# Kernel tuning notes

Measured on AMD Instinct MI355X. Metric: run time of the kernel, lower is better.

Reference implementation:

```python
import jax, jax.numpy as jnp
import numpy as np

N, C, T, V = 32, 64, 256, 25
IC, NS = 16, 3  # inter_channels = C // 4, num_subset = 3
EPS = 1e-5


def _bn(x, g, b, m, v):
    # inference-mode BatchNorm2d over channel dim of [N, C, T, V]
    scale = g / jnp.sqrt(v + EPS)
    return (x - m[:, None, None]) * scale[:, None, None] + b[:, None, None]


def _conv1x1(x, w, b):
    # 1x1 Conv2d on [N, C, T, V]; w: [O, C], b: [O]
    return jnp.einsum('nctv,oc->notv', x, w) + b[None, :, None, None]


def setup_inputs() -> dict:
    key = jax.random.key(0)
    ks = iter(jax.random.split(key, 40))
    def nrm(shape, s=0.05):
        return jax.random.normal(next(ks), shape, jnp.float32) * s
    inp = {}
    inp['feature'] = jax.random.normal(next(ks), (N, C, T, V), jnp.float32)
    inp['hidden'] = jax.random.normal(next(ks), (N, C, T, V), jnp.float32)
    inp['A'] = jax.random.uniform(next(ks), (NS, V, V), jnp.float32) * 0.1
    inp['PA'] = jnp.full((NS, V, V), 1e-6, jnp.float32)
    inp['conv_a_w'] = nrm((NS, IC, C)); inp['conv_a_b'] = nrm((NS, IC))
    inp['conv_b_w'] = nrm((NS, IC, C)); inp['conv_b_b'] = nrm((NS, IC))
    inp['conv_d_w'] = nrm((NS, C, C));  inp['conv_d_b'] = nrm((NS, C))
    inp['gbn_g'] = 0.5 + jax.random.uniform(next(ks), (C,), jnp.float32)
    inp['gbn_b'] = nrm((C,))
    inp['gbn_m'] = nrm((C,))
    inp['gbn_v'] = 0.5 + jax.random.uniform(next(ks), (C,), jnp.float32)
    inp['tcn_w'] = nrm((C, C, 9, 1)); inp['tcn_b'] = nrm((C,))
    inp['tbn_g'] = 0.5 + jax.random.uniform(next(ks), (C,), jnp.float32)
    inp['tbn_b'] = nrm((C,))
    inp['tbn_m'] = nrm((C,))
    inp['tbn_v'] = 0.5 + jax.random.uniform(next(ks), (C,), jnp.float32)
    for nme in ['W_ir', 'W_ii', 'W_in', 'W_hr', 'W_hi', 'W_hh']:
        inp[nme] = nrm((C, C))
    for nme in ['b_ir', 'b_ii', 'b_in']:
        inp[nme] = nrm((C,))
    return inp


def _tcn_gcn(h, A, PA, caw, cab, cbw, cbb, cdw, cdb,
             gbn_g, gbn_b, gbn_m, gbn_v, tcn_w, tcn_b,
             tbn_g, tbn_b, tbn_m, tbn_v):
    # unit_gcn (in == out -> down is identity)
    Aeff = A + PA  # [NS, V, V]
    scale = 1.0 / (IC * T)
    y = 0.0
    h_flat = h.reshape(N, C * T, V)
    for i in range(NS):
        a = _conv1x1(h, caw[i], cab[i])            # [N, IC, T, V]
        b = _conv1x1(h, cbw[i], cbb[i])            # [N, IC, T, V]
        A1 = a.transpose(0, 3, 1, 2).reshape(N, V, IC * T)
        A2 = b.reshape(N, IC * T, V)
        att = jax.nn.softmax(jnp.einsum('nvk,nkw->nvw', A1, A2) * scale, axis=-2)
        att = att + Aeff[i]                         # [N, V, V]
        z = jnp.einsum('nkv,nvw->nkw', h_flat, att).reshape(N, C, T, V)
        y = y + _conv1x1(z, cdw[i], cdb[i])
    gcn_out = jax.nn.relu(_bn(y, gbn_g, gbn_b, gbn_m, gbn_v) + h)
    # unit_tcn: (9,1) conv, pad (4,0), stride 1
    t = jax.lax.conv_general_dilated(
        gcn_out, tcn_w, window_strides=(1, 1), padding=[(4, 4), (0, 0)],
        dimension_numbers=('NCHW', 'OIHW', 'NCHW'))
    t = t + tcn_b[None, :, None, None]
    t = _bn(t, tbn_g, tbn_b, tbn_m, tbn_v)
    # residual is identity (in==out, stride 1)
    return jax.nn.relu(t + h)


def reference(feature, hidden, A, PA, conv_a_w, conv_a_b, conv_b_w, conv_b_b,
              conv_d_w, conv_d_b, gbn_g, gbn_b, gbn_m, gbn_v, tcn_w, tcn_b,
              tbn_g, tbn_b, tbn_m, tbn_v, W_ir, b_ir, W_ii, b_ii, W_in, b_in,
              W_hr, W_hi, W_hh):
    msg = _tcn_gcn(hidden, A, PA, conv_a_w, conv_a_b, conv_b_w, conv_b_b,
                   conv_d_w, conv_d_b, gbn_g, gbn_b, gbn_m, gbn_v,
                   tcn_w, tcn_b, tbn_g, tbn_b, tbn_m, tbn_v)
    feat = feature.transpose(0, 2, 3, 1).reshape(N, T * V, C)
    msg2 = msg.transpose(0, 2, 3, 1).reshape(N, T * V, C)
    hid2 = hidden.transpose(0, 2, 3, 1).reshape(N, T * V, C)
    r = jax.nn.sigmoid(feat @ W_ir.T + b_ir + msg2 @ W_hr.T)
    z = jax.nn.sigmoid(feat @ W_ii.T + b_ii + msg2 @ W_hi.T)
    n = jnp.tanh(feat @ W_in.T + b_in + r * (msg2 @ W_hh.T))
    h_new = (1.0 - z) * n + z * hid2
    return h_new.reshape(N, T, V, C).transpose(0, 3, 1, 2)
```

## Files before the change

kernel.cpp:

```cpp
#include <hip/hip_runtime.h>
#include <math.h>

#define TV 6400
#define NTOT 32

typedef __attribute__((ext_vector_type(8))) short short8;
typedef __attribute__((ext_vector_type(4))) short short4v;
typedef __attribute__((ext_vector_type(4))) float f32x4;

__device__ __forceinline__ float b2f(short s) {
  unsigned u = ((unsigned)(unsigned short)s) << 16;
  return __uint_as_float(u);
}
__device__ __forceinline__ short f2b(float f) {
  unsigned u = __float_as_uint(f);
  u = (u + 0x7FFF + ((u >> 16) & 1)) >> 16;
  return (short)u;
}
__device__ __forceinline__ float fsig(float x) {
  return __builtin_amdgcn_rcpf(1.f + __expf(-x));
}
__device__ __forceinline__ float ftanh(float x) {
  float x2 = fminf(fmaxf(2.f * x, -80.f), 80.f);
  float t = __expf(x2);
  return (t - 1.f) * __builtin_amdgcn_rcpf(t + 1.f);
}

__global__ __launch_bounds__(256) void pack_kernel(
    const float* __restrict__ tcn_w, const float* __restrict__ caw,
    const float* __restrict__ cbw, const float* __restrict__ cdw,
    const float* __restrict__ W_ir, const float* __restrict__ W_ii,
    const float* __restrict__ W_in, const float* __restrict__ W_hr,
    const float* __restrict__ W_hi, const float* __restrict__ W_hh,
    const float* __restrict__ cab, const float* __restrict__ cbb,
    const float* __restrict__ b_ir, const float* __restrict__ b_ii,
    const float* __restrict__ b_in,
    short* __restrict__ P, float* __restrict__ Pb)
{
  int idx = blockIdx.x * 256 + threadIdx.x;
  if (idx < 9984) {
    int lane = idx & 63;
    int rest = idx >> 6;
    int c = rest & 1;
    rest >>= 1;
    int mloc = lane & 15, kb = c * 32 + (lane >> 4) * 8;
    short8 v;
    if (rest < 6) {
      int m = rest * 16 + mloc;
      for (int i = 0; i < 8; ++i)
        v[i] = f2b(m < 48 ? caw[m * 64 + kb + i] : cbw[(m - 48) * 64 + kb + i]);
    } else if (rest < 18) {
      int m = (rest - 6) * 16 + mloc;
      for (int i = 0; i < 8; ++i) v[i] = f2b(cdw[m * 64 + kb + i]);
    } else if (rest < 30) {
      int m = (rest - 18) * 16 + mloc;
      const float* W = (m < 64) ? W_ir : (m < 128 ? W_ii : W_in);
      int mr = m & 63;
      for (int i = 0; i < 8; ++i) v[i] = f2b(W[mr * 64 + kb + i]);
    } else if (rest < 42) {
      int m = (rest - 30) * 16 + mloc;
      const float* W = (m < 64) ? W_hr : (m < 128 ? W_hi : W_hh);
      int mr = m & 63;
      for (int i = 0; i < 8; ++i) v[i] = f2b(W[mr * 64 + kb + i]);
    } else {
      int t = rest - 42;
      int kk = t >> 2, mf = t & 3;
      int o = mf * 16 + mloc;
      for (int i = 0; i < 8; ++i) v[i] = f2b(tcn_w[o * 576 + (kb + i) * 9 + kk]);
    }
    *(short8*)(P + (size_t)idx * 8) = v;
  } else if (idx < 9984 + 288) {
    int r = idx - 9984;
    if (r < 96) Pb[r] = (r < 48) ? cab[r] : cbb[r - 48];
    else {
      int q = r - 96;
      Pb[r] = (q < 64) ? b_ir[q] : (q < 128 ? b_ii[q - 64] : b_in[q - 128]);
    }
  }
}

__global__ __launch_bounds__(256) void convert_kernel(
    const float* __restrict__ hid, const float* __restrict__ feat,
    short* __restrict__ hidK, short* __restrict__ featK)
{
  int j = blockIdx.x * 256 + threadIdx.x;
  int gy = blockIdx.y;
  int n = blockIdx.z;
  const float* src = ((gy < 8) ? hid : feat) + ((long)n * 64 + (long)(gy & 7) * 8) * TV + j;
  short* dst = ((gy < 8) ? hidK : featK) + (((long)n * 8 + (gy & 7)) * TV + j) * 8;
  short8 o;
#pragma unroll
  for (int i = 0; i < 8; ++i) o[i] = f2b(src[(long)i * TV]);
  *(short8*)dst = o;
}

__global__ __launch_bounds__(256) void ab_gemm(
    const short8* __restrict__ Wp, const short8* __restrict__ Bk,
    short* __restrict__ Cout, const float* __restrict__ bias)
{
  const int tid = threadIdx.x;
  const int lane = tid & 63, w = tid >> 6;
  const int q = lane >> 4, lj = lane & 15;
  const int j0 = blockIdx.x * 128;
  const int n = blockIdx.y;
  const short8* Bn = Bk + (long)n * 8 * TV;
  short* Cn = Cout + (long)n * 96 * TV;

  f32x4 acc[6][2];
  for (int a = 0; a < 6; ++a) for (int b = 0; b < 2; ++b)
    acc[a][b] = (f32x4){0.f, 0.f, 0.f, 0.f};

  for (int c = 0; c < 2; ++c) {
    short8 bf0 = Bn[(long)(c * 4 + q) * TV + j0 + (w * 2 + 0) * 16 + lj];
    short8 bf1 = Bn[(long)(c * 4 + q) * TV + j0 + (w * 2 + 1) * 16 + lj];
#pragma unroll
    for (int mf = 0; mf < 6; ++mf) {
      short8 af = Wp[(mf * 2 + c) * 64 + lane];
      acc[mf][0] = __builtin_amdgcn_mfma_f32_16x16x32_bf16(af, bf0, acc[mf][0], 0, 0, 0);
      acc[mf][1] = __builtin_amdgcn_mfma_f32_16x16x32_bf16(af, bf1, acc[mf][1], 0, 0, 0);
    }
  }
#pragma unroll
  for (int mf = 0; mf < 6; ++mf) {
    int k0 = mf * 16 + q * 4;
    int g = k0 >> 3, i0 = k0 & 7;
    float bv[4];
#pragma unroll
    for (int r = 0; r < 4; ++r) bv[r] = bias[k0 + r];
#pragma unroll
    for (int jf = 0; jf < 2; ++jf) {
      int j = j0 + (w * 2 + jf) * 16 + lj;
      short4v o4;
#pragma unroll
      for (int r = 0; r < 4; ++r) o4[r] = f2b(acc[mf][jf][r] + bv[r]);
      *(short4v*)(Cn + ((long)g * TV + j) * 8 + i0) = o4;
    }
  }
}

__global__ __launch_bounds__(256) void att_partial(
    const short* __restrict__ abK, float* __restrict__ partial)
{
  const int ch = blockIdx.x, i = blockIdx.y, n = blockIdx.z;
  __shared__ float sA[6400], sB[6400];
  const int tid = threadIdx.x;
  const long nb = (long)n * 96 * TV;
  const int t0 = ch * 16;
  for (int idx = tid; idx < 800; idx += 256) {
    int gh = idx / 400, jl = idx - gh * 400;
    long j = (long)t0 * 25 + jl;
    short8 va = *(const short8*)&abK[nb + ((long)(2 * i + gh) * TV + j) * 8];
    short8 vb = *(const short8*)&abK[nb + ((long)(6 + 2 * i + gh) * TV + j) * 8];
#pragma unroll
    for (int e = 0; e < 8; ++e) {
      sA[(gh * 8 + e) * 400 + jl] = b2f(va[e]);
      sB[(gh * 8 + e) * 400 + jl] = b2f(vb[e]);
    }
  }
  __syncthreads();
  const int a0 = tid >> 4, b0 = tid & 15;
  const int v1 = a0 + 16, w1 = b0 + 16;
  const int v1c = (v1 < 25) ? v1 : 0, w1c = (w1 < 25) ? w1 : 0;
  float acc00 = 0, acc01 = 0, acc10 = 0, acc11 = 0;
#pragma unroll 8
  for (int r = 0; r < 256; ++r) {
    float av0 = sA[r * 25 + a0], av1 = sA[r * 25 + v1c];
    float bw0 = sB[r * 25 + b0], bw1 = sB[r * 25 + w1c];
    acc00 += av0 * bw0; acc01 += av0 * bw1;
    acc10 += av1 * bw0; acc11 += av1 * bw1;
  }
  const float scale = 1.0f / 4096.0f;
  float* pp = partial + (((long)(n * 3 + i) * 16) + ch) * 625;
  pp[a0 * 25 + b0] = acc00 * scale;
  if (w1 < 25) pp[a0 * 25 + w1] = acc01 * scale;
  if (v1 < 25) pp[v1 * 25 + b0] = acc10 * scale;
  if (v1 < 25 && w1 < 25) pp[v1 * 25 + w1] = acc11 * scale;
}

__global__ __launch_bounds__(256) void att_reduce(
    const float* __restrict__ partial, const float* __restrict__ Amat,
    const float* __restrict__ PAmat, short* __restrict__ attP)
{
  const int i = blockIdx.x, n = blockIdx.y;
  __shared__ float sL[625];
  const int tid = threadIdx.x;
  const float* pp = partial + ((long)(n * 3 + i) * 16) * 625;
  for (int idx = tid; idx < 625; idx += 256) {
    float s = 0.f;
#pragma unroll
    for (int c = 0; c < 16; ++c) s += pp[c * 625 + idx];
    sL[idx] = s;
  }
  __syncthreads();
  if (tid < 25) {
    const int w = tid;
    float mx = -1e30f;
#pragma unroll
    for (int v = 0; v < 25; ++v) mx = fmaxf(mx, sL[v * 25 + w]);
    float e[25];
    float s = 0.f;
#pragma unroll
    for (int v = 0; v < 25; ++v) { e[v] = __expf(sL[v * 25 + w] - mx); s += e[v]; }
    float inv = 1.f / s;
#pragma unroll
    for (int v = 0; v < 25; ++v)
      sL[v * 25 + w] = e[v] * inv + Amat[i * 625 + v * 25 + w] + PAmat[i * 625 + v * 25 + w];
  }
  __syncthreads();
  if (tid < 128) {
    int wf = tid >> 6, lane = tid & 63;
    int q = lane >> 4, lj = lane & 15;
    int w = wf * 16 + lj;
    short8 o = {0, 0, 0, 0, 0, 0, 0, 0};
    if (w < 25) {
#pragma unroll
      for (int e2 = 0; e2 < 8; ++e2) {
        int v = q * 8 + e2;
        if (v < 25) o[e2] = f2b(sL[v * 25 + w]);
      }
    }
    *(short8*)(attP + (size_t)(((long)(n * 3 + i) * 2 + wf) * 64 + lane) * 8) = o;
  }
}

#define UST 136
#define OST 101
__global__ __launch_bounds__(256) void gcn_fused(
    const short8* __restrict__ Wu, const short8* __restrict__ attP,
    const short8* __restrict__ hidK, const float* __restrict__ cdb,
    const float* __restrict__ gg, const float* __restrict__ gb,
    const float* __restrict__ gm, const float* __restrict__ gv,
    short* __restrict__ gcnK)
{
  __shared__ __align__(16) short uT[192 * UST];
  __shared__ float A2[64], B2[64];
  short* sOut = uT;
  const int tid = threadIdx.x;
  if (tid < 64) {
    float sc = gg[tid] * rsqrtf(gv[tid] + 1e-5f);
    A2[tid] = sc;
    float bias = cdb[tid] + cdb[64 + tid] + cdb[128 + tid];
    B2[tid] = bias * sc + (gb[tid] - gm[tid] * sc);
  }
  for (int idx = tid; idx < 5376; idx += 256) {
    int row = idx / 28, rr = idx - row * 28;
    int g = rr / 7, s = 25 + (rr - g * 7);
    uT[row * UST + g * 32 + s] = 0;
  }
  const int lane = tid & 63, w = tid >> 6;
  const int q = lane >> 4, lj = lane & 15;
  const int tt = blockIdx.x, n = blockIdx.y;
  const int jb = tt * 100;
  const short8* Hn = hidK + (long)n * 8 * TV;

  f32x4 uacc[3][7];
  for (int a = 0; a < 3; ++a) for (int b = 0; b < 7; ++b)
    uacc[a][b] = (f32x4){0.f, 0.f, 0.f, 0.f};
  for (int c = 0; c < 2; ++c) {
    short8 bf[7];
#pragma unroll
    for (int jf = 0; jf < 7; ++jf)
      bf[jf] = Hn[(long)(c * 4 + q) * TV + jb + jf * 16 + lj];
#pragma unroll
    for (int ml = 0; ml < 3; ++ml) {
      short8 af = Wu[((w * 3 + ml) * 2 + c) * 64 + lane];
#pragma unroll
      for (int jf = 0; jf < 7; ++jf)
        uacc[ml][jf] = __builtin_amdgcn_mfma_f32_16x16x32_bf16(af, bf[jf], uacc[ml][jf], 0, 0, 0);
    }
  }
#pragma unroll
  for (int ml = 0; ml < 3; ++ml) {
    int row0 = (w * 3 + ml) * 16 + q * 4;
#pragma unroll
    for (int jf = 0; jf < 7; ++jf) {
      int col = jf * 16 + lj;
      if (col < 100) {
        int cc = (col / 25) * 32 + (col % 25);
#pragma unroll
        for (int r = 0; r < 4; ++r)
          uT[(row0 + r) * UST + cc] = f2b(uacc[ml][jf][r]);
      }
    }
  }
  __syncthreads();

  const int colt = w * 25;
  short8 attA[6];
#pragma unroll
  for (int i = 0; i < 3; ++i)
#pragma unroll
    for (int wf = 0; wf < 2; ++wf)
      attA[i * 2 + wf] = attP[((long)(n * 3 + i) * 2 + wf) * 64 + lane];

  f32x4 macc[2][4];
  for (int a = 0; a < 2; ++a) for (int b = 0; b < 4; ++b)
    macc[a][b] = (f32x4){0.f, 0.f, 0.f, 0.f};
#pragma unroll
  for (int i = 0; i < 3; ++i) {
#pragma unroll
    for (int of = 0; of < 4; ++of) {
      int row = i * 64 + of * 16 + lj;
      short8 bf = *(const short8*)&uT[row * UST + w * 32 + q * 8];
      macc[0][of] = __builtin_amdgcn_mfma_f32_16x16x32_bf16(attA[i * 2 + 0], bf, macc[0][of], 0, 0, 0);
      macc[1][of] = __builtin_amdgcn_mfma_f32_16x16x32_bf16(attA[i * 2 + 1], bf, macc[1][of], 0, 0, 0);
    }
  }
  __syncthreads();
#pragma unroll
  for (int wf = 0; wf < 2; ++wf)
#pragma unroll
    for (int of = 0; of < 4; ++of)
#pragma unroll
      for (int r = 0; r < 4; ++r) {
        int wl = wf * 16 + q * 4 + r;
        if (wl < 25)
          sOut[(of * 16 + lj) * OST + colt + wl] = f2b(macc[wf][of][r]);
      }
  __syncthreads();

  const short* HnS = (const short*)Hn;
  short* Gn = gcnK + (long)n * 64 * TV;
  for (int u2 = tid; u2 < 800; u2 += 256) {
    int col = u2 % 100, og = u2 / 100;
    long ubase = ((long)og * TV + jb + col) * 8;
    short8 h8 = *(const short8*)&HnS[ubase];
    short8 o8;
#pragma unroll
    for (int e = 0; e < 8; ++e) {
      int o = og * 8 + e;
      float acc = b2f(sOut[o * OST + col]);
      float vv = fmaxf(acc * A2[o] + B2[o] + b2f(h8[e]), 0.f);
      o8[e] = f2b(vv);
    }
    *(short8*)&Gn[ubase] = o8;
  }
}

__global__ __launch_bounds__(256) void tcn_mfma(
    const short8* __restrict__ wTp, const short8* __restrict__ gcnK,
    const short* __restrict__ hidK, const float* __restrict__ tcn_b,
    const float* __restrict__ pbg, const float* __restrict__ pbb,
    const float* __restrict__ pbm, const float* __restrict__ pbv,
    short* __restrict__ msgK)
{
  __shared__ __align__(16) short8 sW[4608];
  __shared__ float A2[64], B2[64];
  const int tid = threadIdx.x;
  for (int idx = tid; idx < 4608; idx += 256) sW[idx] = wTp[idx];
  if (tid < 64) {
    float sc = pbg[tid] * rsqrtf(pbv[tid] + 1e-5f);
    A2[tid] = sc;
    B2[tid] = tcn_b[tid] * sc + (pbb[tid] - pbm[tid] * sc);
  }
  __syncthreads();
  const int lane = tid & 63, w = tid >> 6;
  const int q = lane >> 4, lj = lane & 15;
  const int j0 = blockIdx.x * 128;
  const int n = blockIdx.y;
  const short8* Bn = gcnK + (long)n * 8 * TV;
  const short8 zero8 = {0, 0, 0, 0, 0, 0, 0, 0};

  f32x4 acc[4][2];
  for (int a = 0; a < 4; ++a) for (int b = 0; b < 2; ++b)
    acc[a][b] = (f32x4){0.f, 0.f, 0.f, 0.f};

  for (int kk = 0; kk < 9; ++kk) {
    const int shift = (kk - 4) * 25;
    for (int c = 0; c < 2; ++c) {
      short8 bfv[2];
#pragma unroll
      for (int jf = 0; jf < 2; ++jf) {
        int col = j0 + (w * 2 + jf) * 16 + lj + shift;
        bool valid = ((unsigned)col < (unsigned)TV);
        short8 t = Bn[(long)(c * 4 + q) * TV + (valid ? col : 0)];
        bfv[jf] = valid ? t : zero8;
      }
#pragma unroll
      for (int mf = 0; mf < 4; ++mf) {
        short8 af = sW[((kk * 4 + mf) * 2 + c) * 64 + lane];
        acc[mf][0] = __builtin_amdgcn_mfma_f32_16x16x32_bf16(af, bfv[0], acc[mf][0], 0, 0, 0);
        acc[mf][1] = __builtin_amdgcn_mfma_f32_16x16x32_bf16(af, bfv[1], acc[mf][1], 0, 0, 0);
      }
    }
  }

  short* Mn = msgK + (long)n * 64 * TV;
  const short* Hn = hidK + (long)n * 64 * TV;
#pragma unroll
  for (int mf = 0; mf < 4; ++mf) {
    int k0 = mf * 16 + q * 4;
    int g = k0 >> 3, i0 = k0 & 7;
#pragma unroll
    for (int jf = 0; jf < 2; ++jf) {
      int j = j0 + (w * 2 + jf) * 16 + lj;
      long base = ((long)g * TV + j) * 8 + i0;
      short4v h4 = *(const short4v*)&Hn[base];
      short4v o4;
#pragma unroll
      for (int r = 0; r < 4; ++r) {
        float v = acc[mf][jf][r] * A2[k0 + r] + B2[k0 + r] + b2f(h4[r]);
        o4[r] = f2b(fmaxf(v, 0.f));
      }
      *(short4v*)&Mn[base] = o4;
    }
  }
}

__global__ __launch_bounds__(256) void gru_mfma(
    const short8* __restrict__ WFp, const short8* __restrict__ WHp,
    const float* __restrict__ bF, const short8* __restrict__ featK,
    const short8* __restrict__ msgK, const short* __restrict__ hidK,
    float* __restrict__ outp)
{
  __shared__ __align__(16) short8 sW[3072];
  __shared__ float sBias[192];
  const int tid = threadIdx.x;
  for (int idx = tid; idx < 1536; idx += 256) {
    sW[idx] = WFp[idx];
    sW[1536 + idx] = WHp[idx];
  }
  if (tid < 192) sBias[tid] = bF[tid];
  __syncthreads();

  const int lane = tid & 63, w = tid >> 6;
  const int q = lane >> 4, lj = lane & 15;
  const int j0 = blockIdx.x * 64;
  const int n = blockIdx.y;
  const int j = j0 + w * 16 + lj;
  const short8* Fn = featK + (long)n * 8 * TV;
  const short8* Mn = msgK + (long)n * 8 * TV;

  f32x4 accF[12], accH[12];
  for (int a = 0; a < 12; ++a) {
    accF[a] = (f32x4){0.f, 0.f, 0.f, 0.f};
    accH[a] = (f32x4){0.f, 0.f, 0.f, 0.f};
  }
  for (int c = 0; c < 2; ++c) {
    short8 bFf = Fn[(long)(c * 4 + q) * TV + j];
    short8 bHf = Mn[(long)(c * 4 + q) * TV + j];
#pragma unroll
    for (int mf = 0; mf < 12; ++mf) {
      short8 af = sW[(mf * 2 + c) * 64 + lane];
      accF[mf] = __builtin_amdgcn_mfma_f32_16x16x32_bf16(af, bFf, accF[mf], 0, 0, 0);
      short8 ah = sW[1536 + (mf * 2 + c) * 64 + lane];
      accH[mf] = __builtin_amdgcn_mfma_f32_16x16x32_bf16(ah, bHf, accH[mf], 0, 0, 0);
    }
  }

  const short* Hn = hidK + (long)n * 64 * TV;
  float* On = outp + (long)n * 64 * TV;
#pragma unroll
  for (int mf = 0; mf < 4; ++mf) {
    int k0 = mf * 16 + q * 4;
    int g = k0 >> 3, i0 = k0 & 7;
    short4v h4 = *(const short4v*)&Hn[((long)g * TV + j) * 8 + i0];
#pragma unroll
    for (int r = 0; r < 4; ++r) {
      int o = k0 + r;
      float rp = accF[mf][r] + sBias[o] + accH[mf][r];
      float zp = accF[mf + 4][r] + sBias[64 + o] + accH[mf + 4][r];
      float np = accF[mf + 8][r] + sBias[128 + o];
      float rv = fsig(rp);
      float zv = fsig(zp);
      float nn = ftanh(np + rv * accH[mf + 8][r]);
      float hv = b2f(h4[r]);
      On[(long)o * TV + j] = (1.f - zv) * nn + zv * hv;
    }
  }
}

extern "C" void kernel_launch(void* const* d_in, const int* in_sizes, int n_in,
                              void* d_out, int out_size, void* d_ws, size_t ws_size,
                              hipStream_t stream)
{
  const float* feature = (const float*)d_in[0];
  const float* hidden  = (const float*)d_in[1];
  const float* Amat    = (const float*)d_in[2];
  const float* PAmat   = (const float*)d_in[3];
  const float* caw = (const float*)d_in[4];
  const float* cab = (const float*)d_in[5];
  const float* cbw = (const float*)d_in[6];
  const float* cbb = (const float*)d_in[7];
  const float* cdw = (const float*)d_in[8];
  const float* cdb = (const float*)d_in[9];
  const float* gbn_g = (const float*)d_in[10];
  const float* gbn_b = (const float*)d_in[11];
  const float* gbn_m = (const float*)d_in[12];
  const float* gbn_v = (const float*)d_in[13];
  const float* tcn_w = (const float*)d_in[14];
  const float* tcn_b = (const float*)d_in[15];
  const float* tbn_g = (const float*)d_in[16];
  const float* tbn_b = (const float*)d_in[17];
  const float* tbn_m = (const float*)d_in[18];
  const float* tbn_v = (const float*)d_in[19];
  const float* W_ir = (const float*)d_in[20];
  const float* W_ii = (const float*)d_in[21];
  const float* W_in = (const float*)d_in[22];
  const float* W_hr = (const float*)d_in[23];
  const float* W_hi = (const float*)d_in[24];
  const float* W_hh = (const float*)d_in[25];
  const float* b_ir = (const float*)d_in[26];
  const float* b_ii = (const float*)d_in[27];
  const float* b_in = (const float*)d_in[28];
  float* out = (float*)d_out;

  int Nc = NTOT;
  while (Nc > 1) {
    size_t need = (size_t)352 * TV * 2 * Nc + (size_t)Nc * 30000 * 4 +
                  (size_t)Nc * 3072 * 2 + 79872 * 2 + 288 * 4 + 4096;
    if (need <= ws_size) break;
    Nc >>= 1;
  }

  char* p = (char*)d_ws;
  short* hidK = (short*)p;  p += (size_t)Nc * 64 * TV * 2;
  short* featK = (short*)p; p += (size_t)Nc * 64 * TV * 2;
  short* abK = (short*)p;   p += (size_t)Nc * 96 * TV * 2;
  short* gcnK = (short*)p;  p += (size_t)Nc * 64 * TV * 2;
  short* msgK = (short*)p;  p += (size_t)Nc * 64 * TV * 2;
  float* partial = (float*)p; p += (size_t)Nc * 30000 * 4;
  short* attP = (short*)p;    p += (size_t)Nc * 3072 * 2;
  p = (char*)(((size_t)p + 15) & ~(size_t)15);
  short* P = (short*)p;       p += 79872 * 2;
  float* Pb = (float*)p;

  pack_kernel<<<dim3(41), dim3(256), 0, stream>>>(
      tcn_w, caw, cbw, cdw, W_ir, W_ii, W_in, W_hr, W_hi, W_hh,
      cab, cbb, b_ir, b_ii, b_in, P, Pb);

  const long s64 = (long)64 * TV;
  for (int c0 = 0; c0 < NTOT; c0 += Nc) {
    const float* hidc = hidden + (long)c0 * s64;
    const float* featc = feature + (long)c0 * s64;
    float* outc = out + (long)c0 * s64;

    convert_kernel<<<dim3(25, 16, Nc), 256, 0, stream>>>(hidc, featc, hidK, featK);
    ab_gemm<<<dim3(50, Nc), 256, 0, stream>>>(
        (const short8*)P, (const short8*)hidK, abK, Pb);
    att_partial<<<dim3(16, 3, Nc), 256, 0, stream>>>(abK, partial);
    att_reduce<<<dim3(3, Nc), 256, 0, stream>>>(partial, Amat, PAmat, attP);
    gcn_fused<<<dim3(64, Nc), 256, 0, stream>>>(
        (const short8*)P + 768, (const short8*)attP, (const short8*)hidK,
        cdb, gbn_g, gbn_b, gbn_m, gbn_v, gcnK);
    tcn_mfma<<<dim3(50, Nc), 256, 0, stream>>>(
        (const short8*)P + 5376, (const short8*)gcnK, hidK, tcn_b,
        tbn_g, tbn_b, tbn_m, tbn_v, msgK);
    gru_mfma<<<dim3(100, Nc), 256, 0, stream>>>(
        (const short8*)P + 2304, (const short8*)P + 3840, Pb + 96,
        (const short8*)featK, (const short8*)msgK, hidK, outc);
  }
}
```

Before: 367.0 us.

## Use MFMA attention kernel, fold feature conversion into GRU, batch TCN over two samples

Replaces the two-stage scalar attention (partial + reduce) with one MFMA-based kernel per (subset, sample) that reduces four wave partials in shared memory. The feature tensor is no longer pre-converted to bf16. The GRU kernel now reads fp32 feature directly and converts it in registers, removing a write and read of a full bf16 copy. The TCN kernel processes two samples per block so each block loads its shared weight tile half as often. Risks: the attention kernel now has only 3*Nc blocks doing a long serial loop, and the strided fp32 feature reads in the GRU kernel may be less efficient.

```diff
diff --git a/kernel.cpp b/kernel.cpp
--- a/kernel.cpp
+++ b/kernel.cpp
@@ -80,14 +80,13 @@
 }
 
 __global__ __launch_bounds__(256) void convert_kernel(
-    const float* __restrict__ hid, const float* __restrict__ feat,
-    short* __restrict__ hidK, short* __restrict__ featK)
+    const float* __restrict__ hid, short* __restrict__ hidK)
 {
   int j = blockIdx.x * 256 + threadIdx.x;
-  int gy = blockIdx.y;
+  int g = blockIdx.y;
   int n = blockIdx.z;
-  const float* src = ((gy < 8) ? hid : feat) + ((long)n * 64 + (long)(gy & 7) * 8) * TV + j;
-  short* dst = ((gy < 8) ? hidK : featK) + (((long)n * 8 + (gy & 7)) * TV + j) * 8;
+  const float* src = hid + ((long)n * 64 + (long)g * 8) * TV + j;
+  short* dst = hidK + (((long)n * 8 + g) * TV + j) * 8;
   short8 o;
 #pragma unroll
   for (int i = 0; i < 8; ++i) o[i] = f2b(src[(long)i * TV]);
@@ -138,88 +137,81 @@
   }
 }
 
-__global__ __launch_bounds__(256) void att_partial(
-    const short* __restrict__ abK, float* __restrict__ partial)
-{
-  const int ch = blockIdx.x, i = blockIdx.y, n = blockIdx.z;
-  __shared__ float sA[6400], sB[6400];
+__global__ __launch_bounds__(256) void att_mfma(
+    const short* __restrict__ abK, const float* __restrict__ Amat,
+    const float* __restrict__ PAmat, short* __restrict__ attP)
+{
+  const int i = blockIdx.x, n = blockIdx.y;
+  __shared__ float sP[4096];
+  __shared__ float sL[640];
   const int tid = threadIdx.x;
-  const long nb = (long)n * 96 * TV;
-  const int t0 = ch * 16;
-  for (int idx = tid; idx < 800; idx += 256) {
-    int gh = idx / 400, jl = idx - gh * 400;
-    long j = (long)t0 * 25 + jl;
-    short8 va = *(const short8*)&abK[nb + ((long)(2 * i + gh) * TV + j) * 8];
-    short8 vb = *(const short8*)&abK[nb + ((long)(6 + 2 * i + gh) * TV + j) * 8];
-#pragma unroll
-    for (int e = 0; e < 8; ++e) {
-      sA[(gh * 8 + e) * 400 + jl] = b2f(va[e]);
-      sB[(gh * 8 + e) * 400 + jl] = b2f(vb[e]);
-    }
-  }
-  __syncthreads();
-  const int a0 = tid >> 4, b0 = tid & 15;
-  const int v1 = a0 + 16, w1 = b0 + 16;
-  const int v1c = (v1 < 25) ? v1 : 0, w1c = (w1 < 25) ? w1 : 0;
-  float acc00 = 0, acc01 = 0, acc10 = 0, acc11 = 0;
-#pragma unroll 8
-  for (int r = 0; r < 256; ++r) {
-    float av0 = sA[r * 25 + a0], av1 = sA[r * 25 + v1c];
-    float bw0 = sB[r * 25 + b0], bw1 = sB[r * 25 + w1c];
-    acc00 += av0 * bw0; acc01 += av0 * bw1;
-    acc10 += av1 * bw0; acc11 += av1 * bw1;
+  const int lane = tid & 63, w = tid >> 6;
+  const int q = lane >> 4, lj = lane & 15;
+  const long nb = (long)n * 12 * TV;
+  const long ga = nb + (long)(2 * i + (q & 1)) * TV;
+  const long gb = nb + (long)(6 + 2 * i + (q & 1)) * TV;
+  const int tq = q >> 1;
+
+  f32x4 acc[2][2];
+  for (int a = 0; a < 2; ++a) for (int b = 0; b < 2; ++b)
+    acc[a][b] = (f32x4){0.f, 0.f, 0.f, 0.f};
+
+  for (int p = w * 32; p < w * 32 + 32; ++p) {
+    long jb = (long)(2 * p + tq) * 25;
+    short8 a0 = *(const short8*)&abK[(ga + jb + lj) * 8];
+    short8 a1 = *(const short8*)&abK[(ga + jb + 16 + lj) * 8];
+    short8 b0 = *(const short8*)&abK[(gb + jb + lj) * 8];
+    short8 b1 = *(const short8*)&abK[(gb + jb + 16 + lj) * 8];
+    acc[0][0] = __builtin_amdgcn_mfma_f32_16x16x32_bf16(a0, b0, acc[0][0], 0, 0, 0);
+    acc[0][1] = __builtin_amdgcn_mfma_f32_16x16x32_bf16(a0, b1, acc[0][1], 0, 0, 0);
+    acc[1][0] = __builtin_amdgcn_mfma_f32_16x16x32_bf16(a1, b0, acc[1][0], 0, 0, 0);
+    acc[1][1] = __builtin_amdgcn_mfma_f32_16x16x32_bf16(a1, b1, acc[1][1], 0, 0, 0);
   }
   const float scale = 1.0f / 4096.0f;
-  float* pp = partial + (((long)(n * 3 + i) * 16) + ch) * 625;
-  pp[a0 * 25 + b0] = acc00 * scale;
-  if (w1 < 25) pp[a0 * 25 + w1] = acc01 * scale;
-  if (v1 < 25) pp[v1 * 25 + b0] = acc10 * scale;
-  if (v1 < 25 && w1 < 25) pp[v1 * 25 + w1] = acc11 * scale;
-}
-
-__global__ __launch_bounds__(256) void att_reduce(
-    const float* __restrict__ partial, const float* __restrict__ Amat,
-    const float* __restrict__ PAmat, short* __restrict__ attP)
-{
-  const int i = blockIdx.x, n = blockIdx.y;
-  __shared__ float sL[625];
-  const int tid = threadIdx.x;
-  const float* pp = partial + ((long)(n * 3 + i) * 16) * 625;
+#pragma unroll
+  for (int mi = 0; mi < 2; ++mi)
+#pragma unroll
+    for (int wi = 0; wi < 2; ++wi)
+#pragma unroll
+      for (int r = 0; r < 4; ++r)
+        sP[w * 1024 + (mi * 16 + q * 4 + r) * 32 + wi * 16 + lj] =
+            acc[mi][wi][r] * scale;
+  __syncthreads();
+
   for (int idx = tid; idx < 625; idx += 256) {
-    float s = 0.f;
-#pragma unroll
-    for (int c = 0; c < 16; ++c) s += pp[c * 625 + idx];
-    sL[idx] = s;
+    int v = idx / 25, w2 = idx - v * 25;
+    int o = v * 32 + w2;
+    sL[idx] = sP[o] + sP[1024 + o] + sP[2048 + o] + sP[3072 + o];
   }
   __syncthreads();
   if (tid < 25) {
-    const int w = tid;
+    const int w2 = tid;
     float mx = -1e30f;
 #pragma unroll
-    for (int v = 0; v < 25; ++v) mx = fmaxf(mx, sL[v * 25 + w]);
+    for (int v = 0; v < 25; ++v) mx = fmaxf(mx, sL[v * 25 + w2]);
     float e[25];
     float s = 0.f;
 #pragma unroll
-    for (int v = 0; v < 25; ++v) { e[v] = __expf(sL[v * 25 + w] - mx); s += e[v]; }
+    for (int v = 0; v < 25; ++v) { e[v] = __expf(sL[v * 25 + w2] - mx); s += e[v]; }
     float inv = 1.f / s;
 #pragma unroll
     for (int v = 0; v < 25; ++v)
-      sL[v * 25 + w] = e[v] * inv + Amat[i * 625 + v * 25 + w] + PAmat[i * 625 + v * 25 + w];
+      sL[v * 25 + w2] = e[v] * inv + Amat[i * 625 + v * 25 + w2] + PAmat[i * 625 + v * 25 + w2];
   }
   __syncthreads();
   if (tid < 128) {
-    int wf = tid >> 6, lane = tid & 63;
-    int q = lane >> 4, lj = lane & 15;
-    int w = wf * 16 + lj;
+    int wf = tid >> 6, lane2 = tid & 63;
+    int q2 = lane2 >> 4, lj2 = lane2 & 15;
+    int w2 = wf * 16 + lj2;
     short8 o = {0, 0, 0, 0, 0, 0, 0, 0};
-    if (w < 25) {
+    if (w2 < 25) {
 #pragma unroll
       for (int e2 = 0; e2 < 8; ++e2) {
-        int v = q * 8 + e2;
-        if (v < 25) o[e2] = f2b(sL[v * 25 + w]);
+        int v = q2 * 8 + e2;
+        if (v < 25) o[e2] = f2b(sL[v * 25 + w2]);
       }
     }
-    *(short8*)(attP + (size_t)(((long)(n * 3 + i) * 2 + wf) * 64 + lane) * 8) = o;
+    *(short8*)(attP + (size_t)(((long)(n * 3 + i) * 2 + wf) * 64 + lane2) * 8) = o;
   }
 }
 
@@ -342,7 +334,7 @@
     const short* __restrict__ hidK, const float* __restrict__ tcn_b,
     const float* __restrict__ pbg, const float* __restrict__ pbb,
     const float* __restrict__ pbm, const float* __restrict__ pbv,
-    short* __restrict__ msgK)
+    short* __restrict__ msgK, int Nchunk)
 {
   __shared__ __align__(16) short8 sW[4608];
   __shared__ float A2[64], B2[64];
@@ -357,59 +349,63 @@
   const int lane = tid & 63, w = tid >> 6;
   const int q = lane >> 4, lj = lane & 15;
   const int j0 = blockIdx.x * 128;
-  const int n = blockIdx.y;
-  const short8* Bn = gcnK + (long)n * 8 * TV;
   const short8 zero8 = {0, 0, 0, 0, 0, 0, 0, 0};
 
-  f32x4 acc[4][2];
-  for (int a = 0; a < 4; ++a) for (int b = 0; b < 2; ++b)
-    acc[a][b] = (f32x4){0.f, 0.f, 0.f, 0.f};
-
-  for (int kk = 0; kk < 9; ++kk) {
-    const int shift = (kk - 4) * 25;
-    for (int c = 0; c < 2; ++c) {
-      short8 bfv[2];
+  for (int ni = 0; ni < 2; ++ni) {
+    const int n = blockIdx.y * 2 + ni;
+    if (n >= Nchunk) break;
+    const short8* Bn = gcnK + (long)n * 8 * TV;
+
+    f32x4 acc[4][2];
+    for (int a = 0; a < 4; ++a) for (int b = 0; b < 2; ++b)
+      acc[a][b] = (f32x4){0.f, 0.f, 0.f, 0.f};
+
+    for (int kk = 0; kk < 9; ++kk) {
+      const int shift = (kk - 4) * 25;
+      for (int c = 0; c < 2; ++c) {
+        short8 bfv[2];
+#pragma unroll
+        for (int jf = 0; jf < 2; ++jf) {
+          int col = j0 + (w * 2 + jf) * 16 + lj + shift;
+          bool valid = ((unsigned)col < (unsigned)TV);
+          short8 t = Bn[(long)(c * 4 + q) * TV + (valid ? col : 0)];
+          bfv[jf] = valid ? t : zero8;
+        }
+#pragma unroll
+        for (int mf = 0; mf < 4; ++mf) {
+          short8 af = sW[((kk * 4 + mf) * 2 + c) * 64 + lane];
+          acc[mf][0] = __builtin_amdgcn_mfma_f32_16x16x32_bf16(af, bfv[0], acc[mf][0], 0, 0, 0);
+          acc[mf][1] = __builtin_amdgcn_mfma_f32_16x16x32_bf16(af, bfv[1], acc[mf][1], 0, 0, 0);
+        }
+      }
+    }
+
+    short* Mn = msgK + (long)n * 64 * TV;
+    const short* Hn = hidK + (long)n * 64 * TV;
+#pragma unroll
+    for (int mf = 0; mf < 4; ++mf) {
+      int k0 = mf * 16 + q * 4;
+      int g = k0 >> 3, i0 = k0 & 7;
 #pragma unroll
       for (int jf = 0; jf < 2; ++jf) {
-        int col = j0 + (w * 2 + jf) * 16 + lj + shift;
-        bool valid = ((unsigned)col < (unsigned)TV);
-        short8 t = Bn[(long)(c * 4 + q) * TV + (valid ? col : 0)];
-        bfv[jf] = valid ? t : zero8;
+        int j = j0 + (w * 2 + jf) * 16 + lj;
+        long base = ((long)g * TV + j) * 8 + i0;
+        short4v h4 = *(const short4v*)&Hn[base];
+        short4v o4;
+#pragma unroll
+        for (int r = 0; r < 4; ++r) {
+          float v = acc[mf][jf][r] * A2[k0 + r] + B2[k0 + r] + b2f(h4[r]);
+          o4[r] = f2b(fmaxf(v, 0.f));
+        }
+        *(short4v*)&Mn[base] = o4;
       }
-#pragma unroll
-      for (int mf = 0; mf < 4; ++mf) {
-        short8 af = sW[((kk * 4 + mf) * 2 + c) * 64 + lane];
-        acc[mf][0] = __builtin_amdgcn_mfma_f32_16x16x32_bf16(af, bfv[0], acc[mf][0], 0, 0, 0);
-        acc[mf][1] = __builtin_amdgcn_mfma_f32_16x16x32_bf16(af, bfv[1], acc[mf][1], 0, 0, 0);
-      }
-    }
-  }
-
-  short* Mn = msgK + (long)n * 64 * TV;
-  const short* Hn = hidK + (long)n * 64 * TV;
-#pragma unroll
-  for (int mf = 0; mf < 4; ++mf) {
-    int k0 = mf * 16 + q * 4;
-    int g = k0 >> 3, i0 = k0 & 7;
-#pragma unroll
-    for (int jf = 0; jf < 2; ++jf) {
-      int j = j0 + (w * 2 + jf) * 16 + lj;
-      long base = ((long)g * TV + j) * 8 + i0;
-      short4v h4 = *(const short4v*)&Hn[base];
-      short4v o4;
-#pragma unroll
-      for (int r = 0; r < 4; ++r) {
-        float v = acc[mf][jf][r] * A2[k0 + r] + B2[k0 + r] + b2f(h4[r]);
-        o4[r] = f2b(fmaxf(v, 0.f));
-      }
-      *(short4v*)&Mn[base] = o4;
     }
   }
 }
 
 __global__ __launch_bounds__(256) void gru_mfma(
     const short8* __restrict__ WFp, const short8* __restrict__ WHp,
-    const float* __restrict__ bF, const short8* __restrict__ featK,
+    const float* __restrict__ bF, const float* __restrict__ feat,
     const short8* __restrict__ msgK, const short* __restrict__ hidK,
     float* __restrict__ outp)
 {
@@ -428,7 +424,7 @@
   const int j0 = blockIdx.x * 64;
   const int n = blockIdx.y;
   const int j = j0 + w * 16 + lj;
-  const short8* Fn = featK + (long)n * 8 * TV;
+  const float* Ffn = feat + (long)n * 64 * TV;
   const short8* Mn = msgK + (long)n * 8 * TV;
 
   f32x4 accF[12], accH[12];
@@ -437,7 +433,10 @@
     accH[a] = (f32x4){0.f, 0.f, 0.f, 0.f};
   }
   for (int c = 0; c < 2; ++c) {
-    short8 bFf = Fn[(long)(c * 4 + q) * TV + j];
+    short8 bFf;
+#pragma unroll
+    for (int e = 0; e < 8; ++e)
+      bFf[e] = f2b(Ffn[(long)(c * 32 + q * 8 + e) * TV + j]);
     short8 bHf = Mn[(long)(c * 4 + q) * TV + j];
 #pragma unroll
     for (int mf = 0; mf < 12; ++mf) {
@@ -507,22 +506,20 @@
 
   int Nc = NTOT;
   while (Nc > 1) {
-    size_t need = (size_t)352 * TV * 2 * Nc + (size_t)Nc * 30000 * 4 +
-                  (size_t)Nc * 3072 * 2 + 79872 * 2 + 288 * 4 + 4096;
+    size_t need = (size_t)288 * TV * 2 * Nc + (size_t)Nc * 3072 * 2 +
+                  79872 * 2 + 288 * 4 + 4096;
     if (need <= ws_size) break;
     Nc >>= 1;
   }
 
   char* p = (char*)d_ws;
   short* hidK = (short*)p;  p += (size_t)Nc * 64 * TV * 2;
-  short* featK = (short*)p; p += (size_t)Nc * 64 * TV * 2;
   short* abK = (short*)p;   p += (size_t)Nc * 96 * TV * 2;
   short* gcnK = (short*)p;  p += (size_t)Nc * 64 * TV * 2;
   short* msgK = (short*)p;  p += (size_t)Nc * 64 * TV * 2;
-  float* partial = (float*)p; p += (size_t)Nc * 30000 * 4;
-  short* attP = (short*)p;    p += (size_t)Nc * 3072 * 2;
+  short* attP = (short*)p;  p += (size_t)Nc * 3072 * 2;
   p = (char*)(((size_t)p + 15) & ~(size_t)15);
-  short* P = (short*)p;       p += 79872 * 2;
+  short* P = (short*)p;     p += 79872 * 2;
   float* Pb = (float*)p;
 
   pack_kernel<<<dim3(41), dim3(256), 0, stream>>>(
@@ -535,19 +532,18 @@
     const float* featc = feature + (long)c0 * s64;
     float* outc = out + (long)c0 * s64;
 
-    convert_kernel<<<dim3(25, 16, Nc), 256, 0, stream>>>(hidc, featc, hidK, featK);
+    convert_kernel<<<dim3(25, 8, Nc), 256, 0, stream>>>(hidc, hidK);
     ab_gemm<<<dim3(50, Nc), 256, 0, stream>>>(
         (const short8*)P, (const short8*)hidK, abK, Pb);
-    att_partial<<<dim3(16, 3, Nc), 256, 0, stream>>>(abK, partial);
-    att_reduce<<<dim3(3, Nc), 256, 0, stream>>>(partial, Amat, PAmat, attP);
+    att_mfma<<<dim3(3, Nc), 256, 0, stream>>>(abK, Amat, PAmat, attP);
     gcn_fused<<<dim3(64, Nc), 256, 0, stream>>>(
         (const short8*)P + 768, (const short8*)attP, (const short8*)hidK,
         cdb, gbn_g, gbn_b, gbn_m, gbn_v, gcnK);
-    tcn_mfma<<<dim3(50, Nc), 256, 0, stream>>>(
+    tcn_mfma<<<dim3(50, (Nc + 1) / 2), 256, 0, stream>>>(
         (const short8*)P + 5376, (const short8*)gcnK, hidK, tcn_b,
-        tbn_g, tbn_b, tbn_m, tbn_v, msgK);
+        tbn_g, tbn_b, tbn_m, tbn_v, msgK, Nc);
     gru_mfma<<<dim3(100, Nc), 256, 0, stream>>>(
         (const short8*)P + 2304, (const short8*)P + 3840, Pb + 96,
-        (const short8*)featK, (const short8*)msgK, hidK, outc);
-  }
-}
+        featc, (const short8*)msgK, hidK, outc);
+  }
+}
```

After: 348.7 us. 1.05x faster.
